# Kernel tuning notes

Measured on AMD Instinct MI355X. Metric: run time of the kernel, lower is better.

Reference implementation:

```python
import jax, jax.numpy as jnp
import numpy as np

N = 50000      # nodes
E = 400000     # edges per edge type
T = 4          # edge types: add/sub/mul/div
F_IN = 128     # in_channels
H = 2          # heads
C = 64         # hidden_channels (per head)
HC = H * C     # 128
MLP = C // 8   # hidden_channels // 8 = 8
NUM_CLASSES = 10


def _glorot(key, shape):
    fan_in, fan_out = shape[-2], shape[-1]
    s = jnp.sqrt(6.0 / (fan_in + fan_out))
    return jax.random.uniform(key, shape, jnp.float32, -s, s)


def setup_inputs() -> dict:
    key = jax.random.key(0)
    ks = jax.random.split(key, 12)
    x = jax.random.normal(ks[0], (N, F_IN), jnp.float32)
    edge_index = jax.random.randint(ks[1], (T, 2, E), 0, N, jnp.int32)
    # layer-1 GATv2 params, stacked over the 4 edge types
    Wl1 = _glorot(ks[2], (T, F_IN, HC))
    Wr1 = _glorot(ks[3], (T, F_IN, HC))
    att1 = _glorot(ks[4], (T, H, C))
    b1 = jnp.zeros((T, HC), jnp.float32)
    # layer-2 GATv2 params (input dim = hidden*heads)
    Wl2 = _glorot(ks[5], (T, HC, HC))
    Wr2 = _glorot(ks[6], (T, HC, HC))
    att2 = _glorot(ks[7], (T, H, C))
    b2 = jnp.zeros((T, HC), jnp.float32)
    # MLP head
    W_lin1 = _glorot(ks[8], (HC, MLP))
    b_lin1 = jnp.zeros((MLP,), jnp.float32)
    W_lin2 = _glorot(ks[9], (MLP, NUM_CLASSES))
    b_lin2 = jnp.zeros((NUM_CLASSES,), jnp.float32)
    return dict(x=x, edge_index=edge_index, Wl1=Wl1, Wr1=Wr1, att1=att1, b1=b1,
                Wl2=Wl2, Wr2=Wr2, att2=att2, b2=b2,
                W_lin1=W_lin1, b_lin1=b_lin1, W_lin2=W_lin2, b_lin2=b_lin2)


def gatv2_conv(x, src, dst, Wl, Wr, att, bias):
    """PyG GATv2Conv: add self-loops, per-edge LeakyReLU attention,
    softmax over incoming edges per destination, weighted scatter-add."""
    n = x.shape[0]
    xl = (x @ Wl).reshape(n, H, C)   # source transform
    xr = (x @ Wr).reshape(n, H, C)   # destination transform
    loop = jnp.arange(n, dtype=src.dtype)
    s = jnp.concatenate([src, loop])
    d = jnp.concatenate([dst, loop])
    e = jax.nn.leaky_relu(xl[s] + xr[d], 0.2)          # [E+n, H, C]
    score = jnp.einsum('ehc,hc->eh', e, att)           # [E+n, H]
    smax = jax.ops.segment_max(score, d, num_segments=n)  # [N, H]
    p = jnp.exp(score - smax[d])                       # stable softmax numerators
    denom = jax.ops.segment_sum(p, d, num_segments=n)  # [N, H]
    msg = jax.ops.segment_sum(p[:, :, None] * xl[s], d, num_segments=n)  # [N, H, C]
    out = msg / denom[:, :, None]
    return out.reshape(n, HC) + bias


def hetero_layer(x, edge_index, Wl, Wr, att, b):
    # HeteroConv with aggr='sum' over the 4 edge types (single node type)
    out = gatv2_conv(x, edge_index[0, 0], edge_index[0, 1], Wl[0], Wr[0], att[0], b[0])
    for t in range(1, T):
        out = out + gatv2_conv(x, edge_index[t, 0], edge_index[t, 1], Wl[t], Wr[t], att[t], b[t])
    return out


def reference(x, edge_index, Wl1, Wr1, att1, b1, Wl2, Wr2, att2, b2,
              W_lin1, b_lin1, W_lin2, b_lin2):
    h = jax.nn.relu(hetero_layer(x, edge_index, Wl1, Wr1, att1, b1))
    h = jax.nn.relu(hetero_layer(h, edge_index, Wl2, Wr2, att2, b2))
    h = jax.nn.relu(h @ W_lin1 + b_lin1)
    # dropout p=0.5 is identity at eval time
    return h @ W_lin2 + b_lin2
```

## Files before the change

kernel.cpp:

```cpp
#include <hip/hip_runtime.h>
#include <hip/hip_bf16.h>
#include <math.h>

#define NN 50000
#define EE 400000
#define EEN 450000
#define TT 4
#define FD 128
#define RPS 50004
#define NBKT 196
#define BCAP 4096
#define LOG2E 1.44269504f

typedef __attribute__((ext_vector_type(8))) short bf16x8;
typedef __attribute__((ext_vector_type(4))) float f32x4;

__device__ inline float bf2f(unsigned short u) {
  union { unsigned int i; float f; } x; x.i = ((unsigned int)u) << 16; return x.f;
}
__device__ inline unsigned short f2bf(float f) {
  __hip_bfloat16 h = __float2bfloat16(f);
  unsigned short u; __builtin_memcpy(&u, &h, 2); return u;
}
__device__ inline float blo(unsigned int u) {
  union { unsigned int i; float f; } x; x.i = u << 16; return x.f;
}
__device__ inline float bhi(unsigned int u) {
  union { unsigned int i; float f; } x; x.i = u & 0xFFFF0000u; return x.f;
}
__device__ inline float fexp2(float x) { return __builtin_amdgcn_exp2f(x); }
__device__ inline float sgn04(float a) {
  union { float f; unsigned int i; } x; x.f = a;
  x.i = (x.i & 0x80000000u) | 0x3ECCCCCDu;
  return x.f;
}
__device__ inline float qsum8(float v) {
  v += __builtin_bit_cast(float, __builtin_amdgcn_update_dpp(
         0, __builtin_bit_cast(int, v), 0xB1, 0xF, 0xF, true));
  v += __builtin_bit_cast(float, __builtin_amdgcn_update_dpp(
         0, __builtin_bit_cast(int, v), 0x4E, 0xF, 0xF, true));
  v += __builtin_bit_cast(float, __builtin_amdgcn_update_dpp(
         0, __builtin_bit_cast(int, v), 0x141, 0xF, 0xF, true));
  return v;
}
__device__ inline void unpack8(const uint4 u, float* x) {
  x[0] = blo(u.x); x[1] = bhi(u.x); x[2] = blo(u.y); x[3] = bhi(u.y);
  x[4] = blo(u.z); x[5] = bhi(u.z); x[6] = blo(u.w); x[7] = bhi(u.w);
}

__global__ void k_cvtW(const float* __restrict__ Wl1, const float* __restrict__ Wr1,
                       const float* __restrict__ Wl2, const float* __restrict__ Wr2,
                       unsigned short* __restrict__ Bpack) {
  const int idx = blockIdx.x * 256 + threadIdx.x;
  const int R = idx >> 14;
  const int kc = idx & 16383;
  const int lr = R & 1, t = (R >> 1) & 3, layer = R >> 3;
  const float* W = layer ? (lr ? Wr2 : Wl2) : (lr ? Wr1 : Wl1);
  const float v = W[t * 16384 + kc];
  const int k = kc >> 7, c = kc & 127;
  const int nt = c >> 4, ks = k >> 5, g = (k >> 3) & 3, j = k & 7;
  const int lane = g * 16 + (c & 15);
  Bpack[(size_t)R * 16384 + ((nt * 4 + ks) * 64 + lane) * 8 + j] = f2bf(v);
}

__global__ void k_cvtA(const float* __restrict__ src, unsigned short* __restrict__ ahi,
                       unsigned short* __restrict__ alo) {
  const int idx = blockIdx.x * 256 + threadIdx.x;
  float4 v = ((const float4*)src)[idx];
  const unsigned short h0 = f2bf(v.x), h1 = f2bf(v.y), h2 = f2bf(v.z), h3 = f2bf(v.w);
  const unsigned short l0 = f2bf(v.x - bf2f(h0)), l1 = f2bf(v.y - bf2f(h1));
  const unsigned short l2 = f2bf(v.z - bf2f(h2)), l3 = f2bf(v.w - bf2f(h3));
  uint2 hv, lv;
  hv.x = (unsigned)h0 | ((unsigned)h1 << 16); hv.y = (unsigned)h2 | ((unsigned)h3 << 16);
  lv.x = (unsigned)l0 | ((unsigned)l1 << 16); lv.y = (unsigned)l2 | ((unsigned)l3 << 16);
  ((uint2*)ahi)[idx] = hv;
  ((uint2*)alo)[idx] = lv;
}

__global__ __launch_bounds__(128) void k_gemm4(
    const unsigned short* __restrict__ Ahi, const unsigned short* __restrict__ Alo,
    const unsigned short* __restrict__ Bbase,
    unsigned short* __restrict__ xl4, unsigned short* __restrict__ xr4) {
  const int t = blockIdx.y;
  const unsigned short* Bpt = Bbase + (size_t)t * 2 * 16384;
  unsigned short* xl = xl4 + (size_t)t * NN * FD;
  unsigned short* xr = xr4 + (size_t)t * NN * FD;
  const int tid = threadIdx.x;
  const int lane = tid & 63;
  const int w = tid >> 6;
  const int rh = lane & 15, g = lane >> 4;
  const int m0 = blockIdx.x * 64 + w * 32;
  f32x4 acc[2][16];
  #pragma unroll
  for (int a = 0; a < 2; ++a)
    #pragma unroll
    for (int b = 0; b < 16; ++b) acc[a][b] = (f32x4){0.f, 0.f, 0.f, 0.f};
  int r0 = m0 + rh;      if (r0 > NN - 1) r0 = NN - 1;
  int r1 = m0 + 16 + rh; if (r1 > NN - 1) r1 = NN - 1;
  #pragma unroll
  for (int ks = 0; ks < 4; ++ks) {
    const int ko = ks * 32 + g * 8;
    const bf16x8 ah0 = *(const bf16x8*)(Ahi + (size_t)r0 * FD + ko);
    const bf16x8 al0 = *(const bf16x8*)(Alo + (size_t)r0 * FD + ko);
    const bf16x8 ah1 = *(const bf16x8*)(Ahi + (size_t)r1 * FD + ko);
    const bf16x8 al1 = *(const bf16x8*)(Alo + (size_t)r1 * FD + ko);
    #pragma unroll
    for (int nt = 0; nt < 16; ++nt) {
      const bf16x8 b = *(const bf16x8*)(Bpt + (nt >> 3) * 16384 +
                                        (((nt & 7) * 4 + ks) * 64 + lane) * 8);
      acc[0][nt] = __builtin_amdgcn_mfma_f32_16x16x32_bf16(ah0, b, acc[0][nt], 0, 0, 0);
      acc[0][nt] = __builtin_amdgcn_mfma_f32_16x16x32_bf16(al0, b, acc[0][nt], 0, 0, 0);
      acc[1][nt] = __builtin_amdgcn_mfma_f32_16x16x32_bf16(ah1, b, acc[1][nt], 0, 0, 0);
      acc[1][nt] = __builtin_amdgcn_mfma_f32_16x16x32_bf16(al1, b, acc[1][nt], 0, 0, 0);
    }
  }
  #pragma unroll
  for (int mt = 0; mt < 2; ++mt)
    #pragma unroll
    for (int nt = 0; nt < 16; ++nt) {
      unsigned short* op = (nt < 8) ? xl : xr;
      const int cb = (nt & 7) * 16 + rh;
      #pragma unroll
      for (int r = 0; r < 4; ++r) {
        const int row = m0 + mt * 16 + g * 4 + r;
        if (row < NN) op[(size_t)row * FD + cb] = f2bf(acc[mt][nt][r]);
      }
    }
}

__global__ __launch_bounds__(256) void k_bucket(const int* __restrict__ ei,
                                                int* __restrict__ bcur,
                                                unsigned int* __restrict__ ebuf) {
  __shared__ int lcnt[NBKT], lbase[NBKT];
  const int t = blockIdx.y, tid = threadIdx.x;
  const int cbase = blockIdx.x * 4096;
  if (tid < NBKT) lcnt[tid] = 0;
  __syncthreads();
  const int* srcp = ei + (size_t)t * 2 * EE;
  const int* dstp = srcp + EE;
  unsigned int pk[16]; int rk[16];
  #pragma unroll
  for (int i = 0; i < 16; ++i) {
    const int e = cbase + i * 256 + tid;
    rk[i] = -1;
    if (e < EEN) {
      int s, dd;
      if (e < EE) { s = srcp[e]; dd = dstp[e]; }
      else        { s = dd = e - EE; }
      const int b = dd >> 8;
      pk[i] = ((unsigned)dd << 16) | (unsigned)s;
      rk[i] = (atomicAdd(&lcnt[b], 1) << 8) | b;
    }
  }
  __syncthreads();
  if (tid < NBKT && lcnt[tid] > 0) lbase[tid] = atomicAdd(&bcur[t * NBKT + tid], lcnt[tid]);
  __syncthreads();
  #pragma unroll
  for (int i = 0; i < 16; ++i) {
    if (rk[i] >= 0) {
      const int b = rk[i] & 255, r = rk[i] >> 8;
      ebuf[((size_t)t * NBKT + b) * BCAP + lbase[b] + r] = pk[i];
    }
  }
}

__global__ void k_bktscan(const int* __restrict__ bcur, int* __restrict__ bbase) {
  __shared__ int s[TT * NBKT];
  const int tid = threadIdx.x;
  int v0 = 0;
  if (tid < TT * NBKT) { v0 = bcur[tid]; s[tid] = v0; }
  __syncthreads();
  #pragma unroll
  for (int off = 1; off < NBKT; off <<= 1) {
    int a = 0;
    if (tid < TT * NBKT && (tid % NBKT) >= off) a = s[tid - off];
    __syncthreads();
    if (tid < TT * NBKT) s[tid] += a;
    __syncthreads();
  }
  if (tid < TT * NBKT) bbase[tid] = s[tid] - v0;
}

__global__ __launch_bounds__(256) void k_scatter3(const unsigned int* __restrict__ ebuf,
                                                  const int* __restrict__ bcur,
                                                  const int* __restrict__ bbase,
                                                  int* __restrict__ rowp,
                                                  int* __restrict__ col) {
  __shared__ int lc[256], sc[256];
  const int b = blockIdx.x, t = blockIdx.y, tid = threadIdx.x;
  const int d0 = b << 8;
  const int nd = (NN - d0 < 256) ? (NN - d0) : 256;
  const int cnt = bcur[t * NBKT + b];
  const int base = bbase[t * NBKT + b];
  const unsigned int* eb = ebuf + ((size_t)t * NBKT + b) * BCAP;
  lc[tid] = 0;
  __syncthreads();
  for (int j = tid; j < cnt; j += 256) {
    atomicAdd(&lc[(eb[j] >> 16) - d0], 1);
  }
  __syncthreads();
  const int v = lc[tid];
  sc[tid] = v;
  __syncthreads();
  #pragma unroll
  for (int off = 1; off < 256; off <<= 1) {
    const int a = (tid >= off) ? sc[tid - off] : 0;
    __syncthreads();
    sc[tid] += a;
    __syncthreads();
  }
  const int excl = base + sc[tid] - v;
  if (tid < nd) rowp[(size_t)t * RPS + d0 + tid] = excl;
  if (b == NBKT - 1 && tid == 0) rowp[(size_t)t * RPS + NN] = EEN;
  lc[tid] = excl;
  __syncthreads();
  for (int j = tid; j < cnt; j += 256) {
    const unsigned int u = eb[j];
    const int pos = atomicAdd(&lc[(u >> 16) - d0], 1);
    col[(size_t)t * EEN + pos] = (int)(u & 0xFFFF);
  }
}

__global__ __launch_bounds__(256) void k_agg6(
    const unsigned short* __restrict__ xl4, const unsigned short* __restrict__ xr4,
    const int* __restrict__ col, const int* __restrict__ rowp,
    const float* __restrict__ att, const float* __restrict__ bias,
    unsigned short* __restrict__ ahi, unsigned short* __restrict__ alo,
    float* __restrict__ hout, const int mode) {
  const int lane = threadIdx.x & 63;
  const int d = blockIdx.x * 4 + (threadIdx.x >> 6);
  const int g = lane >> 3;
  const int slot = g >> 1, head = g & 1, sub = lane & 7;
  const int laneoff = head * 128 + sub * 16;
  const int choff = head * 64 + sub * 8;
  float o[8];
  #pragma unroll
  for (int j = 0; j < 8; ++j) o[j] = 0.f;
  #pragma unroll
  for (int t = 0; t < TT; ++t) {
    const char* xlt = (const char*)xl4 + (size_t)t * NN * 256 + laneoff;
    const char* xrt = (const char*)xr4 + (size_t)t * NN * 256 + laneoff;
    const int* colt = col + (size_t)t * EEN;
    const float4 a0 = *(const float4*)(att + t * FD + choff);
    const float4 a1 = *(const float4*)(att + t * FD + choff + 4);
    float av[8] = {a0.x, a0.y, a0.z, a0.w, a1.x, a1.y, a1.z, a1.w};
    const uint4 ur = *(const uint4*)(xrt + (size_t)d * 256);
    float xrv[8]; unpack8(ur, xrv);
    float sa[8], axr[8];
    #pragma unroll
    for (int j = 0; j < 8; ++j) {
      av[j] *= LOG2E; sa[j] = sgn04(av[j]); axr[j] = av[j] * xrv[j];
    }
    float den = 0.f, acc[8];
    #pragma unroll
    for (int j = 0; j < 8; ++j) acc[j] = 0.f;
    const int beg = rowp[t * RPS + d];
    const int end = rowp[t * RPS + d + 1];
    for (int e0 = beg; e0 < end; e0 += 4) {
      const int e = e0 + slot;
      const bool act = e < end;
      const int s = colt[act ? e : end - 1];
      const uint4 u = *(const uint4*)(xlt + ((size_t)((unsigned)s << 8)));
      float x[8]; unpack8(u, x);
      float s06 = 0.f, sr = 0.f;
      #pragma unroll
      for (int j = 0; j < 8; ++j) {
        const float q = fmaf(av[j], x[j], axr[j]);
        s06 += q;
        sr = fmaf(sa[j], fabsf(q), sr);
      }
      const float c = qsum8(fmaf(0.6f, s06, sr));
      const float w = act ? fexp2(c) : 0.f;
      den += w;
      #pragma unroll
      for (int j = 0; j < 8; ++j) acc[j] = fmaf(w, x[j], acc[j]);
    }
    den += __shfl_xor(den, 16);
    den += __shfl_xor(den, 32);
    const float rden = __builtin_amdgcn_rcpf(den);
    #pragma unroll
    for (int j = 0; j < 8; ++j) o[j] = fmaf(acc[j], rden, o[j]);
  }
  #pragma unroll
  for (int j = 0; j < 8; ++j) {
    o[j] += __shfl_xor(o[j], 16);
    o[j] += __shfl_xor(o[j], 32);
  }
  #pragma unroll
  for (int t = 0; t < TT; ++t) {
    const float4 b0 = *(const float4*)(bias + t * FD + choff);
    const float4 b1 = *(const float4*)(bias + t * FD + choff + 4);
    o[0] += b0.x; o[1] += b0.y; o[2] += b0.z; o[3] += b0.w;
    o[4] += b1.x; o[5] += b1.y; o[6] += b1.z; o[7] += b1.w;
  }
  if (lane < 16) {
    if (mode == 0) {
      unsigned short hs[8], ls[8];
      #pragma unroll
      for (int j = 0; j < 8; ++j) {
        const float r = fmaxf(o[j], 0.f);
        hs[j] = f2bf(r);
        ls[j] = f2bf(r - bf2f(hs[j]));
      }
      uint4 hv, lv;
      hv.x = (unsigned)hs[0] | ((unsigned)hs[1] << 16);
      hv.y = (unsigned)hs[2] | ((unsigned)hs[3] << 16);
      hv.z = (unsigned)hs[4] | ((unsigned)hs[5] << 16);
      hv.w = (unsigned)hs[6] | ((unsigned)hs[7] << 16);
      lv.x = (unsigned)ls[0] | ((unsigned)ls[1] << 16);
      lv.y = (unsigned)ls[2] | ((unsigned)ls[3] << 16);
      lv.z = (unsigned)ls[4] | ((unsigned)ls[5] << 16);
      lv.w = (unsigned)ls[6] | ((unsigned)ls[7] << 16);
      *(uint4*)((char*)ahi + (size_t)d * 256 + laneoff) = hv;
      *(uint4*)((char*)alo + (size_t)d * 256 + laneoff) = lv;
    } else {
      *(float4*)(hout + (size_t)d * FD + choff) = make_float4(o[0], o[1], o[2], o[3]);
      *(float4*)(hout + (size_t)d * FD + choff + 4) = make_float4(o[4], o[5], o[6], o[7]);
    }
  }
}

__global__ __launch_bounds__(256) void k_mlp(const float* __restrict__ h,
                                             const float* __restrict__ W1,
                                             const float* __restrict__ b1,
                                             const float* __restrict__ W2,
                                             const float* __restrict__ b2,
                                             float* __restrict__ out) {
  __shared__ float sW1[128 * 8];
  __shared__ float sW2[8 * 10];
  __shared__ float sb1[8], sb2[10];
  for (int i = threadIdx.x; i < 1024; i += 256) sW1[i] = W1[i];
  if (threadIdx.x < 80) sW2[threadIdx.x] = W2[threadIdx.x];
  if (threadIdx.x < 8)  sb1[threadIdx.x] = b1[threadIdx.x];
  if (threadIdx.x < 10) sb2[threadIdx.x] = b2[threadIdx.x];
  __syncthreads();
  const int n = blockIdx.x * 256 + threadIdx.x;
  if (n >= NN) return;
  const float* hn = h + (size_t)n * FD;
  float z[8];
  #pragma unroll
  for (int j = 0; j < 8; ++j) z[j] = sb1[j];
  for (int k = 0; k < FD; k += 4) {
    float4 hv = *(const float4*)(hn + k);
    hv.x = fmaxf(hv.x, 0.f); hv.y = fmaxf(hv.y, 0.f);
    hv.z = fmaxf(hv.z, 0.f); hv.w = fmaxf(hv.w, 0.f);
    #pragma unroll
    for (int j = 0; j < 8; ++j) {
      z[j] += hv.x * sW1[(k + 0) * 8 + j] + hv.y * sW1[(k + 1) * 8 + j]
            + hv.z * sW1[(k + 2) * 8 + j] + hv.w * sW1[(k + 3) * 8 + j];
    }
  }
  #pragma unroll
  for (int j = 0; j < 8; ++j) z[j] = fmaxf(z[j], 0.f);
  float o[10];
  #pragma unroll
  for (int c = 0; c < 10; ++c) o[c] = sb2[c];
  #pragma unroll
  for (int j = 0; j < 8; ++j)
    #pragma unroll
    for (int c = 0; c < 10; ++c) o[c] += z[j] * sW2[j * 10 + c];
  float* op = out + (size_t)n * 10;
  #pragma unroll
  for (int c = 0; c < 10; ++c) op[c] = o[c];
}

extern "C" void kernel_launch(void* const* d_in, const int* in_sizes, int n_in,
                              void* d_out, int out_size, void* d_ws, size_t ws_size,
                              hipStream_t stream) {
  const float* x    = (const float*)d_in[0];
  const int*   ei   = (const int*)d_in[1];
  const float* Wl1  = (const float*)d_in[2];
  const float* Wr1  = (const float*)d_in[3];
  const float* att1 = (const float*)d_in[4];
  const float* b1   = (const float*)d_in[5];
  const float* Wl2  = (const float*)d_in[6];
  const float* Wr2  = (const float*)d_in[7];
  const float* att2 = (const float*)d_in[8];
  const float* b2   = (const float*)d_in[9];
  const float* Wi1  = (const float*)d_in[10];
  const float* bi1  = (const float*)d_in[11];
  const float* Wi2  = (const float*)d_in[12];
  const float* bi2  = (const float*)d_in[13];
  float* out = (float*)d_out;

  char* ws = (char*)d_ws;
  size_t off = 0;
  auto alloc = [&](size_t bytes) {
    void* p = ws + off;
    off = (off + bytes + 255) & ~(size_t)255;
    return p;
  };
  unsigned short* xl4   = (unsigned short*)alloc((size_t)TT * NN * FD * 2);
  unsigned short* xr4   = (unsigned short*)alloc((size_t)TT * NN * FD * 2);
  unsigned short* Ahi   = (unsigned short*)alloc((size_t)NN * FD * 2);
  unsigned short* Alo   = (unsigned short*)alloc((size_t)NN * FD * 2);
  unsigned short* Bpack = (unsigned short*)alloc((size_t)2 * TT * 2 * 16384 * 2);
  int*            col   = (int*)alloc((size_t)TT * EEN * 4);
  int*            rowp  = (int*)alloc((size_t)TT * RPS * 4);
  int*            bcur  = (int*)alloc((size_t)TT * NBKT * 4);
  int*            bbase = (int*)alloc((size_t)TT * NBKT * 4);
  unsigned int*   ebuf  = (unsigned int*)alloc((size_t)TT * NBKT * BCAP * 4);
  float* h2 = (float*)Ahi;

  hipMemsetAsync(bcur, 0, (size_t)TT * NBKT * 4, stream);
  k_cvtW<<<1024, 256, 0, stream>>>(Wl1, Wr1, Wl2, Wr2, Bpack);
  k_bucket<<<dim3(110, TT), 256, 0, stream>>>(ei, bcur, ebuf);
  k_bktscan<<<1, 1024, 0, stream>>>(bcur, bbase);
  k_scatter3<<<dim3(NBKT, TT), 256, 0, stream>>>(ebuf, bcur, bbase, rowp, col);

  k_cvtA<<<6250, 256, 0, stream>>>(x, Ahi, Alo);
  k_gemm4<<<dim3(782, TT), 128, 0, stream>>>(Ahi, Alo, Bpack, xl4, xr4);
  k_agg6<<<12500, 256, 0, stream>>>(xl4, xr4, col, rowp, att1, b1,
                                    Ahi, Alo, nullptr, 0);
  k_gemm4<<<dim3(782, TT), 128, 0, stream>>>(Ahi, Alo, Bpack + (size_t)TT * 2 * 16384,
                                             xl4, xr4);
  k_agg6<<<12500, 256, 0, stream>>>(xl4, xr4, col, rowp, att2, b2,
                                    nullptr, nullptr, h2, 1);
  k_mlp<<<(NN + 255) / 256, 256, 0, stream>>>(h2, Wi1, bi1, Wi2, bi2, out);
}
```

Baseline: 646.8 us.

## Remap aggregation to 2 channels per lane with prefetched neighbor rows

The GATv2 aggregation kernel changes its lane mapping. Before, each wave handled 4 edges at once with 8 channels per lane. Now each wave walks edges one at a time with all 64 lanes covering the 128 channels, 2 per lane. Column indices for 4 edges are loaded at once and broadcast with readlane, and the next group of neighbor rows is prefetched into registers while the current group is processed. This drops the cross-slot shuffle reductions and leaves fewer idle lanes on low-degree nodes. In exchange each edge needs a 32-lane reduction (DPP plus swizzle) and uses narrower 4-byte gathers instead of 16-byte ones.

```diff
diff --git a/kernel.cpp b/kernel.cpp
--- a/kernel.cpp
+++ b/kernel.cpp
@@ -34,18 +34,18 @@
   x.i = (x.i & 0x80000000u) | 0x3ECCCCCDu;
   return x.f;
 }
-__device__ inline float qsum8(float v) {
+__device__ inline float qsum32(float v) {
   v += __builtin_bit_cast(float, __builtin_amdgcn_update_dpp(
          0, __builtin_bit_cast(int, v), 0xB1, 0xF, 0xF, true));
   v += __builtin_bit_cast(float, __builtin_amdgcn_update_dpp(
          0, __builtin_bit_cast(int, v), 0x4E, 0xF, 0xF, true));
   v += __builtin_bit_cast(float, __builtin_amdgcn_update_dpp(
          0, __builtin_bit_cast(int, v), 0x141, 0xF, 0xF, true));
+  v += __builtin_bit_cast(float, __builtin_amdgcn_update_dpp(
+         0, __builtin_bit_cast(int, v), 0x140, 0xF, 0xF, true));
+  v += __builtin_bit_cast(float, __builtin_amdgcn_ds_swizzle(
+         __builtin_bit_cast(int, v), 0x401F));
   return v;
-}
-__device__ inline void unpack8(const uint4 u, float* x) {
-  x[0] = blo(u.x); x[1] = bhi(u.x); x[2] = blo(u.y); x[3] = bhi(u.y);
-  x[4] = blo(u.z); x[5] = bhi(u.z); x[6] = blo(u.w); x[7] = bhi(u.w);
 }
 
 __global__ void k_cvtW(const float* __restrict__ Wl1, const float* __restrict__ Wr1,
@@ -221,7 +221,7 @@
   }
 }
 
-__global__ __launch_bounds__(256) void k_agg6(
+__global__ __launch_bounds__(256) void k_agg7(
     const unsigned short* __restrict__ xl4, const unsigned short* __restrict__ xr4,
     const int* __restrict__ col, const int* __restrict__ rowp,
     const float* __restrict__ att, const float* __restrict__ bias,
@@ -229,94 +229,72 @@
     float* __restrict__ hout, const int mode) {
   const int lane = threadIdx.x & 63;
   const int d = blockIdx.x * 4 + (threadIdx.x >> 6);
-  const int g = lane >> 3;
-  const int slot = g >> 1, head = g & 1, sub = lane & 7;
-  const int laneoff = head * 128 + sub * 16;
-  const int choff = head * 64 + sub * 8;
-  float o[8];
-  #pragma unroll
-  for (int j = 0; j < 8; ++j) o[j] = 0.f;
+  const int half = lane >> 5, sub = lane & 31;
+  const int byteoff = half * 128 + sub * 4;
+  const int choff = half * 64 + sub * 2;
+  float o0 = 0.f, o1 = 0.f;
   #pragma unroll
   for (int t = 0; t < TT; ++t) {
-    const char* xlt = (const char*)xl4 + (size_t)t * NN * 256 + laneoff;
-    const char* xrt = (const char*)xr4 + (size_t)t * NN * 256 + laneoff;
+    const char* xlt = (const char*)xl4 + (size_t)t * NN * 256;
+    const char* xrt = (const char*)xr4 + (size_t)t * NN * 256;
     const int* colt = col + (size_t)t * EEN;
-    const float4 a0 = *(const float4*)(att + t * FD + choff);
-    const float4 a1 = *(const float4*)(att + t * FD + choff + 4);
-    float av[8] = {a0.x, a0.y, a0.z, a0.w, a1.x, a1.y, a1.z, a1.w};
-    const uint4 ur = *(const uint4*)(xrt + (size_t)d * 256);
-    float xrv[8]; unpack8(ur, xrv);
-    float sa[8], axr[8];
-    #pragma unroll
-    for (int j = 0; j < 8; ++j) {
-      av[j] *= LOG2E; sa[j] = sgn04(av[j]); axr[j] = av[j] * xrv[j];
-    }
-    float den = 0.f, acc[8];
-    #pragma unroll
-    for (int j = 0; j < 8; ++j) acc[j] = 0.f;
+    float2 av = *(const float2*)(att + t * FD + choff);
+    av.x *= LOG2E; av.y *= LOG2E;
+    const float sa0 = sgn04(av.x), sa1 = sgn04(av.y);
+    const unsigned int ur =
+        *(const unsigned int*)(xrt + (size_t)d * 256 + byteoff);
+    const float axr0 = av.x * blo(ur), axr1 = av.y * bhi(ur);
+    float den = 0.f, ac0 = 0.f, ac1 = 0.f;
     const int beg = rowp[t * RPS + d];
     const int end = rowp[t * RPS + d + 1];
-    for (int e0 = beg; e0 < end; e0 += 4) {
-      const int e = e0 + slot;
-      const bool act = e < end;
-      const int s = colt[act ? e : end - 1];
-      const uint4 u = *(const uint4*)(xlt + ((size_t)((unsigned)s << 8)));
-      float x[8]; unpack8(u, x);
-      float s06 = 0.f, sr = 0.f;
+
+    unsigned int xA[4], xB[4];
+    auto fetch = [&](int e0, unsigned int* xv) {
+      int ci = e0 + (lane & 3);
+      ci = (ci < end) ? ci : (end - 1);
+      const int cvec = colt[ci];
       #pragma unroll
-      for (int j = 0; j < 8; ++j) {
-        const float q = fmaf(av[j], x[j], axr[j]);
-        s06 += q;
-        sr = fmaf(sa[j], fabsf(q), sr);
+      for (int j = 0; j < 4; ++j) {
+        const int c = __builtin_amdgcn_readlane(cvec, j);
+        xv[j] = *(const unsigned int*)(xlt + ((size_t)((unsigned)c << 8)) + byteoff);
       }
-      const float c = qsum8(fmaf(0.6f, s06, sr));
-      const float w = act ? fexp2(c) : 0.f;
-      den += w;
+    };
+    fetch(beg, xA);
+    for (int e = beg; e < end; e += 4) {
+      if (e + 4 < end) fetch(e + 4, xB);
       #pragma unroll
-      for (int j = 0; j < 8; ++j) acc[j] = fmaf(w, x[j], acc[j]);
-    }
-    den += __shfl_xor(den, 16);
-    den += __shfl_xor(den, 32);
+      for (int j = 0; j < 4; ++j) {
+        const float x0 = blo(xA[j]), x1 = bhi(xA[j]);
+        const float q0 = fmaf(av.x, x0, axr0), q1 = fmaf(av.y, x1, axr1);
+        const float r = fmaf(sa1, fabsf(q1), sa0 * fabsf(q0));
+        const float c = qsum32(fmaf(0.6f, q0 + q1, r));
+        const float w = (e + j < end) ? fexp2(c) : 0.f;
+        den += w;
+        ac0 = fmaf(w, x0, ac0);
+        ac1 = fmaf(w, x1, ac1);
+      }
+      #pragma unroll
+      for (int j = 0; j < 4; ++j) xA[j] = xB[j];
+    }
     const float rden = __builtin_amdgcn_rcpf(den);
-    #pragma unroll
-    for (int j = 0; j < 8; ++j) o[j] = fmaf(acc[j], rden, o[j]);
-  }
-  #pragma unroll
-  for (int j = 0; j < 8; ++j) {
-    o[j] += __shfl_xor(o[j], 16);
-    o[j] += __shfl_xor(o[j], 32);
+    o0 = fmaf(ac0, rden, o0);
+    o1 = fmaf(ac1, rden, o1);
   }
   #pragma unroll
   for (int t = 0; t < TT; ++t) {
-    const float4 b0 = *(const float4*)(bias + t * FD + choff);
-    const float4 b1 = *(const float4*)(bias + t * FD + choff + 4);
-    o[0] += b0.x; o[1] += b0.y; o[2] += b0.z; o[3] += b0.w;
-    o[4] += b1.x; o[5] += b1.y; o[6] += b1.z; o[7] += b1.w;
-  }
-  if (lane < 16) {
-    if (mode == 0) {
-      unsigned short hs[8], ls[8];
-      #pragma unroll
-      for (int j = 0; j < 8; ++j) {
-        const float r = fmaxf(o[j], 0.f);
-        hs[j] = f2bf(r);
-        ls[j] = f2bf(r - bf2f(hs[j]));
-      }
-      uint4 hv, lv;
-      hv.x = (unsigned)hs[0] | ((unsigned)hs[1] << 16);
-      hv.y = (unsigned)hs[2] | ((unsigned)hs[3] << 16);
-      hv.z = (unsigned)hs[4] | ((unsigned)hs[5] << 16);
-      hv.w = (unsigned)hs[6] | ((unsigned)hs[7] << 16);
-      lv.x = (unsigned)ls[0] | ((unsigned)ls[1] << 16);
-      lv.y = (unsigned)ls[2] | ((unsigned)ls[3] << 16);
-      lv.z = (unsigned)ls[4] | ((unsigned)ls[5] << 16);
-      lv.w = (unsigned)ls[6] | ((unsigned)ls[7] << 16);
-      *(uint4*)((char*)ahi + (size_t)d * 256 + laneoff) = hv;
-      *(uint4*)((char*)alo + (size_t)d * 256 + laneoff) = lv;
-    } else {
-      *(float4*)(hout + (size_t)d * FD + choff) = make_float4(o[0], o[1], o[2], o[3]);
-      *(float4*)(hout + (size_t)d * FD + choff + 4) = make_float4(o[4], o[5], o[6], o[7]);
-    }
+    const float2 bv = *(const float2*)(bias + t * FD + choff);
+    o0 += bv.x; o1 += bv.y;
+  }
+  if (mode == 0) {
+    o0 = fmaxf(o0, 0.f); o1 = fmaxf(o1, 0.f);
+    const unsigned short h0 = f2bf(o0), h1 = f2bf(o1);
+    const unsigned short l0 = f2bf(o0 - bf2f(h0)), l1 = f2bf(o1 - bf2f(h1));
+    *(unsigned int*)((char*)ahi + (size_t)d * 256 + byteoff) =
+        (unsigned)h0 | ((unsigned)h1 << 16);
+    *(unsigned int*)((char*)alo + (size_t)d * 256 + byteoff) =
+        (unsigned)l0 | ((unsigned)l1 << 16);
+  } else {
+    *(float2*)(hout + (size_t)d * FD + choff) = make_float2(o0, o1);
   }
 }
 
@@ -410,11 +388,11 @@
 
   k_cvtA<<<6250, 256, 0, stream>>>(x, Ahi, Alo);
   k_gemm4<<<dim3(782, TT), 128, 0, stream>>>(Ahi, Alo, Bpack, xl4, xr4);
-  k_agg6<<<12500, 256, 0, stream>>>(xl4, xr4, col, rowp, att1, b1,
+  k_agg7<<<12500, 256, 0, stream>>>(xl4, xr4, col, rowp, att1, b1,
                                     Ahi, Alo, nullptr, 0);
   k_gemm4<<<dim3(782, TT), 128, 0, stream>>>(Ahi, Alo, Bpack + (size_t)TT * 2 * 16384,
                                              xl4, xr4);
-  k_agg6<<<12500, 256, 0, stream>>>(xl4, xr4, col, rowp, att2, b2,
+  k_agg7<<<12500, 256, 0, stream>>>(xl4, xr4, col, rowp, att2, b2,
                                     nullptr, nullptr, h2, 1);
   k_mlp<<<(NN + 255) / 256, 256, 0, stream>>>(h2, Wi1, bi1, Wi2, bi2, out);
 }
```

New measurement: 533.2 us. -17.6%, faster.
